# Kernel tuning notes

Hardware: AMD Instinct MI355X
Metric: run time of the kernel (lower is better)

The kernel has to match this reference:

```python
import jax, jax.numpy as jnp
import numpy as np
from jax import lax

GUARD_CELLS = 80
BG_CELLS = 80
ALPHA = 1.8
CFAR_UNITS = 1 + 2 * GUARD_CELLS + 2 * BG_CELLS          # 321
GUARD_UNITS = 2 * GUARD_CELLS + 1                         # 161
BG_AREA = CFAR_UNITS ** 2 - GUARD_UNITS ** 2              # background ring cell count
FRONT_DIV = (GUARD_UNITS ** 2) * ALPHA


def box_sum(x, k):
    """Same-padded KxK box sum over NCHW x (C=1), via separable 1D convs.

    Mathematically identical to a Conv2d with all-ones KxK kernel, zero bias,
    padding (k-1)//2 -- but O(N*K) instead of O(N*K^2).
    """
    p = (k - 1) // 2
    kh = jnp.ones((1, 1, k, 1), x.dtype)  # OIHW
    kw = jnp.ones((1, 1, 1, k), x.dtype)
    y = lax.conv_general_dilated(x, kh, window_strides=(1, 1), padding=[(p, p), (0, 0)])
    y = lax.conv_general_dilated(y, kw, window_strides=(1, 1), padding=[(0, 0), (p, p)])
    return y


def setup_inputs() -> dict:
    key = jax.random.key(0)
    x = jax.random.uniform(key, (4, 1, 1024, 1024), dtype=jnp.float32)
    return {"x": x}


def reference(x) -> jnp.ndarray:
    allsum = box_sum(x, CFAR_UNITS)            # conv1: 321x321 ones box
    front = box_sum(x, GUARD_UNITS)            # conv2: 161x161 ones box
    back = (allsum - front) / jnp.float32(BG_AREA)     # div1: 1x1 conv = scale
    front = front / jnp.float32(FRONT_DIV)             # div2: 1x1 conv = scale
    return front / back
```

## Files before the change

kernel.cpp:

```cpp
#include <hip/hip_runtime.h>
#include <hip/hip_bf16.h>


#define IMG 4
#define H 1024
#define W 1024
#define NSEG 32
#define SEGR 32
#define PADL 164
#define PADR 164
#define ROWLEN (PADL + W + PADR)

__global__ __launch_bounds__(256) void hbox_kernel(const float* __restrict__ x,
                                                   float* __restrict__ h161,
                                                   float* __restrict__ h321) {
    __shared__ float P[4][ROWLEN];
    const int wave = threadIdx.x >> 6;
    const int lane = threadIdx.x & 63;
    const int row  = (blockIdx.x << 2) + wave;

    const float4* xr = reinterpret_cast<const float4*>(x + (size_t)row * W);
    float v[16];
    {
        float4 a0 = xr[(lane << 2) + 0];
        float4 a1 = xr[(lane << 2) + 1];
        float4 a2 = xr[(lane << 2) + 2];
        float4 a3 = xr[(lane << 2) + 3];
        v[0]=a0.x; v[1]=a0.y; v[2]=a0.z; v[3]=a0.w;
        v[4]=a1.x; v[5]=a1.y; v[6]=a1.z; v[7]=a1.w;
        v[8]=a2.x; v[9]=a2.y; v[10]=a2.z; v[11]=a2.w;
        v[12]=a3.x; v[13]=a3.y; v[14]=a3.z; v[15]=a3.w;
    }
    float s = 0.f;
#pragma unroll
    for (int j = 0; j < 16; ++j) { s += v[j]; v[j] = s; }
    float t = s;
#pragma unroll
    for (int d = 1; d < 64; d <<= 1) {
        float u = __shfl_up(t, d, 64);
        if (lane >= d) t += u;
    }
    const float off = t - s;
#pragma unroll
    for (int j = 0; j < 16; ++j) v[j] += off;
    const float tot = __shfl(t, 63, 64);

    float* rowP = P[wave];
    float4* Pr = reinterpret_cast<float4*>(rowP + PADL);
    Pr[(lane << 2) + 0] = make_float4(v[0], v[1], v[2], v[3]);
    Pr[(lane << 2) + 1] = make_float4(v[4], v[5], v[6], v[7]);
    Pr[(lane << 2) + 2] = make_float4(v[8], v[9], v[10], v[11]);
    Pr[(lane << 2) + 3] = make_float4(v[12], v[13], v[14], v[15]);
    {
        float4* Pz = reinterpret_cast<float4*>(rowP);
        if (lane < 41) {
            Pz[lane]       = make_float4(0.f, 0.f, 0.f, 0.f);
            Pz[297 + lane] = make_float4(tot, tot, tot, tot);
        }
    }
    __syncthreads();

    const float* Pw = &P[wave][PADL];
    float* o161 = h161 + (size_t)row * W;
    float* o321 = h321 + (size_t)row * W;
#pragma unroll
    for (int k = 0; k < 16; ++k) {
        const int c = lane + (k << 6);
        const float s1 = Pw[c + 80]  - Pw[c - 81];
        const float s3 = Pw[c + 160] - Pw[c - 161];
        o161[c] = s1;
        o321[c] = s3;
    }
}

__global__ __launch_bounds__(256) void vscan_kernel(float* __restrict__ h161,
                                                    float* __restrict__ h321,
                                                    float* __restrict__ Btot) {
    const int bx  = blockIdx.x;
    const int img = bx >> 7;
    const int b7  = bx & 127;
    const int seg = b7 >> 2;
    const int cb  = b7 & 3;
    const int col = (cb << 8) + threadIdx.x;
    const int r0  = seg << 5;

    float* p = (blockIdx.y ? h321 : h161) + ((size_t)img << 20) + col;
    float sum = 0.f;
#pragma unroll
    for (int jj = 0; jj < SEGR; jj += 8) {
        float a[8];
#pragma unroll
        for (int j = 0; j < 8; ++j) a[j] = p[(size_t)(r0 + jj + j) << 10];
#pragma unroll
        for (int j = 0; j < 8; ++j) { sum += a[j]; a[j] = sum; }
#pragma unroll
        for (int j = 0; j < 8; ++j) p[(size_t)(r0 + jj + j) << 10] = a[j];
    }
    Btot[((((size_t)blockIdx.y << 2) + img) << 15) + ((size_t)seg << 10) + col] = sum;
}

__global__ __launch_bounds__(256) void segscan_kernel(const float* __restrict__ Btot,
                                                      float* __restrict__ SP) {
    const int t = blockIdx.x * 256 + threadIdx.x;
    const size_t base = ((size_t)(t >> 10) << 15) + (t & 1023);
    const float* b = Btot + base;
    float* sp = SP + base;
    float off = 0.f;
#pragma unroll
    for (int sg = 0; sg < NSEG; ++sg) {
        const float v = b[(size_t)sg << 10];
        sp[(size_t)sg << 10] = off;
        off += v;
    }
}

__global__ __launch_bounds__(512) void final_kernel(const float* __restrict__ g161,
                                                    const float* __restrict__ g321,
                                                    const float* __restrict__ SP,
                                                    float* __restrict__ out) {
    const int img = blockIdx.x >> 9;
    const int r   = ((blockIdx.x & 511) << 1) + (threadIdx.x >> 8);
    const int c4  = threadIdx.x & 255;

    const float4* P1 = reinterpret_cast<const float4*>(g161 + ((size_t)img << 20));
    const float4* P3 = reinterpret_cast<const float4*>(g321 + ((size_t)img << 20));
    const float4* SP1 = reinterpret_cast<const float4*>(SP) + ((size_t)img << 13);
    const float4* SP3 = reinterpret_cast<const float4*>(SP) + ((size_t)(IMG + img) << 13);

    const int hi1 = min(r + 80, H - 1),  lo1 = r - 81;
    const int hi3 = min(r + 160, H - 1), lo3 = r - 161;

    float4 f  = P1[((size_t)hi1 << 8) + c4];
    float4 fs = SP1[(((size_t)hi1 >> 5) << 8) + c4];
    float fx = f.x + fs.x, fy = f.y + fs.y, fz = f.z + fs.z, fw = f.w + fs.w;
    if (lo1 >= 0) {
        float4 g  = P1[((size_t)lo1 << 8) + c4];
        float4 gs = SP1[(((size_t)lo1 >> 5) << 8) + c4];
        fx -= g.x + gs.x; fy -= g.y + gs.y; fz -= g.z + gs.z; fw -= g.w + gs.w;
    }
    float4 a  = P3[((size_t)hi3 << 8) + c4];
    float4 as = SP3[(((size_t)hi3 >> 5) << 8) + c4];
    float ax = a.x + as.x, ay = a.y + as.y, az = a.z + as.z, aw = a.w + as.w;
    if (lo3 >= 0) {
        float4 g  = P3[((size_t)lo3 << 8) + c4];
        float4 gs = SP3[(((size_t)lo3 >> 5) << 8) + c4];
        ax -= g.x + gs.x; ay -= g.y + gs.y; az -= g.z + gs.z; aw -= g.w + gs.w;
    }

    const float SCALE = (float)(77120.0 / 46657.8);
    float4 o;
    o.x = SCALE * fx * __builtin_amdgcn_rcpf(ax - fx);
    o.y = SCALE * fy * __builtin_amdgcn_rcpf(ay - fy);
    o.z = SCALE * fz * __builtin_amdgcn_rcpf(az - fz);
    o.w = SCALE * fw * __builtin_amdgcn_rcpf(aw - fw);
    reinterpret_cast<float4*>(out + ((size_t)img << 20) + ((size_t)r << 10))[c4] = o;
}

extern "C" void kernel_launch(void* const* d_in, const int* in_sizes, int n_in,
                              void* d_out, int out_size, void* d_ws, size_t ws_size,
                              hipStream_t stream) {
    const float* x = (const float*)d_in[0];
    float* outp = (float*)d_out;
    float* h161 = (float*)d_ws;
    float* h321 = h161 + (size_t)IMG * H * W;
    float* Btot = h321 + (size_t)IMG * H * W;
    float* SPb  = Btot + (size_t)2 * IMG * NSEG * W;

    hbox_kernel<<<dim3((IMG * H) / 4), dim3(256), 0, stream>>>(x, h161, h321);
    vscan_kernel<<<dim3(512, 2), dim3(256), 0, stream>>>(h161, h321, Btot);
    segscan_kernel<<<dim3(32), dim3(256), 0, stream>>>(Btot, SPb);
    final_kernel<<<dim3(IMG * (H / 2)), dim3(512), 0, stream>>>(h161, h321, SPb, outp);
}
```

Baseline: 95.30 us.

## Store intermediate box sums as interleaved fp16 pairs to halve traffic

```diff
diff --git a/kernel.cpp b/kernel.cpp
--- a/kernel.cpp
+++ b/kernel.cpp
@@ -1,5 +1,6 @@
 #include <hip/hip_runtime.h>
 #include <hip/hip_bf16.h>
+#include <hip/hip_fp16.h>
 
 
 #define IMG 4
@@ -11,9 +12,11 @@
 #define PADR 164
 #define ROWLEN (PADL + W + PADR)
 
+struct h2x4 { __half2 v[4]; };
+struct f2x4 { float2  v[4]; };
+
 __global__ __launch_bounds__(256) void hbox_kernel(const float* __restrict__ x,
-                                                   float* __restrict__ h161,
-                                                   float* __restrict__ h321) {
+                                                   __half2* __restrict__ hs) {
     __shared__ float P[4][ROWLEN];
     const int wave = threadIdx.x >> 6;
     const int lane = threadIdx.x & 63;
@@ -61,21 +64,18 @@
     __syncthreads();
 
     const float* Pw = &P[wave][PADL];
-    float* o161 = h161 + (size_t)row * W;
-    float* o321 = h321 + (size_t)row * W;
+    __half2* oh = hs + (size_t)row * W;
 #pragma unroll
     for (int k = 0; k < 16; ++k) {
         const int c = lane + (k << 6);
         const float s1 = Pw[c + 80]  - Pw[c - 81];
         const float s3 = Pw[c + 160] - Pw[c - 161];
-        o161[c] = s1;
-        o321[c] = s3;
+        oh[c] = __floats2half2_rn(s1, s3);
     }
 }
 
-__global__ __launch_bounds__(256) void vscan_kernel(float* __restrict__ h161,
-                                                    float* __restrict__ h321,
-                                                    float* __restrict__ Btot) {
+__global__ __launch_bounds__(256) void vscan_kernel(__half2* __restrict__ hs,
+                                                    float2* __restrict__ Btot) {
     const int bx  = blockIdx.x;
     const int img = bx >> 7;
     const int b7  = bx & 127;
@@ -84,75 +84,85 @@
     const int col = (cb << 8) + threadIdx.x;
     const int r0  = seg << 5;
 
-    float* p = (blockIdx.y ? h321 : h161) + ((size_t)img << 20) + col;
-    float sum = 0.f;
+    __half2* p = hs + ((size_t)img << 20) + ((size_t)r0 << 10) + col;
+    float a1 = 0.f, a3 = 0.f;
 #pragma unroll
     for (int jj = 0; jj < SEGR; jj += 8) {
-        float a[8];
+        __half2 hv[8];
 #pragma unroll
-        for (int j = 0; j < 8; ++j) a[j] = p[(size_t)(r0 + jj + j) << 10];
+        for (int j = 0; j < 8; ++j) hv[j] = p[(size_t)(jj + j) << 10];
 #pragma unroll
-        for (int j = 0; j < 8; ++j) { sum += a[j]; a[j] = sum; }
-#pragma unroll
-        for (int j = 0; j < 8; ++j) p[(size_t)(r0 + jj + j) << 10] = a[j];
+        for (int j = 0; j < 8; ++j) {
+            const float2 f = __half22float2(hv[j]);
+            a1 += f.x; a3 += f.y;
+            p[(size_t)(jj + j) << 10] = __floats2half2_rn(a1, a3);
+        }
     }
-    Btot[((((size_t)blockIdx.y << 2) + img) << 15) + ((size_t)seg << 10) + col] = sum;
+    Btot[(((size_t)img * NSEG + seg) << 10) + col] = make_float2(a1, a3);
 }
 
-__global__ __launch_bounds__(256) void segscan_kernel(const float* __restrict__ Btot,
-                                                      float* __restrict__ SP) {
-    const int t = blockIdx.x * 256 + threadIdx.x;
-    const size_t base = ((size_t)(t >> 10) << 15) + (t & 1023);
-    const float* b = Btot + base;
-    float* sp = SP + base;
-    float off = 0.f;
+__global__ __launch_bounds__(256) void segscan_kernel(const float2* __restrict__ Btot,
+                                                      float2* __restrict__ SP) {
+    const int t   = blockIdx.x * 256 + threadIdx.x;
+    const int img = t >> 10;
+    const int col = t & 1023;
+    const float2* b  = Btot + ((size_t)img * NSEG << 10) + col;
+    float2*       sp = SP   + ((size_t)img * NSEG << 10) + col;
+    float o1 = 0.f, o3 = 0.f;
 #pragma unroll
     for (int sg = 0; sg < NSEG; ++sg) {
-        const float v = b[(size_t)sg << 10];
-        sp[(size_t)sg << 10] = off;
-        off += v;
+        const float2 v = b[(size_t)sg << 10];
+        sp[(size_t)sg << 10] = make_float2(o1, o3);
+        o1 += v.x; o3 += v.y;
     }
 }
 
-__global__ __launch_bounds__(512) void final_kernel(const float* __restrict__ g161,
-                                                    const float* __restrict__ g321,
-                                                    const float* __restrict__ SP,
+__global__ __launch_bounds__(512) void final_kernel(const __half2* __restrict__ hs,
+                                                    const float2* __restrict__ SP,
                                                     float* __restrict__ out) {
     const int img = blockIdx.x >> 9;
     const int r   = ((blockIdx.x & 511) << 1) + (threadIdx.x >> 8);
     const int c4  = threadIdx.x & 255;
+    const int cb  = c4 << 2;
 
-    const float4* P1 = reinterpret_cast<const float4*>(g161 + ((size_t)img << 20));
-    const float4* P3 = reinterpret_cast<const float4*>(g321 + ((size_t)img << 20));
-    const float4* SP1 = reinterpret_cast<const float4*>(SP) + ((size_t)img << 13);
-    const float4* SP3 = reinterpret_cast<const float4*>(SP) + ((size_t)(IMG + img) << 13);
+    const __half2* Hi = hs + ((size_t)img << 20);
+    const float2*  Si = SP + ((size_t)img * NSEG << 10);
 
     const int hi1 = min(r + 80, H - 1),  lo1 = r - 81;
     const int hi3 = min(r + 160, H - 1), lo3 = r - 161;
 
-    float4 f  = P1[((size_t)hi1 << 8) + c4];
-    float4 fs = SP1[(((size_t)hi1 >> 5) << 8) + c4];
-    float fx = f.x + fs.x, fy = f.y + fs.y, fz = f.z + fs.z, fw = f.w + fs.w;
+    float fx[4], ax[4];
+    {
+        const h2x4 Hh = *reinterpret_cast<const h2x4*>(Hi + ((size_t)hi1 << 10) + cb);
+        const f2x4 Sh = *reinterpret_cast<const f2x4*>(Si + (((size_t)hi1 >> 5) << 10) + cb);
+#pragma unroll
+        for (int i = 0; i < 4; ++i) fx[i] = __half22float2(Hh.v[i]).x + Sh.v[i].x;
+    }
     if (lo1 >= 0) {
-        float4 g  = P1[((size_t)lo1 << 8) + c4];
-        float4 gs = SP1[(((size_t)lo1 >> 5) << 8) + c4];
-        fx -= g.x + gs.x; fy -= g.y + gs.y; fz -= g.z + gs.z; fw -= g.w + gs.w;
+        const h2x4 Hl = *reinterpret_cast<const h2x4*>(Hi + ((size_t)lo1 << 10) + cb);
+        const f2x4 Sl = *reinterpret_cast<const f2x4*>(Si + (((size_t)lo1 >> 5) << 10) + cb);
+#pragma unroll
+        for (int i = 0; i < 4; ++i) fx[i] -= __half22float2(Hl.v[i]).x + Sl.v[i].x;
     }
-    float4 a  = P3[((size_t)hi3 << 8) + c4];
-    float4 as = SP3[(((size_t)hi3 >> 5) << 8) + c4];
-    float ax = a.x + as.x, ay = a.y + as.y, az = a.z + as.z, aw = a.w + as.w;
+    {
+        const h2x4 Hh = *reinterpret_cast<const h2x4*>(Hi + ((size_t)hi3 << 10) + cb);
+        const f2x4 Sh = *reinterpret_cast<const f2x4*>(Si + (((size_t)hi3 >> 5) << 10) + cb);
+#pragma unroll
+        for (int i = 0; i < 4; ++i) ax[i] = __half22float2(Hh.v[i]).y + Sh.v[i].y;
+    }
     if (lo3 >= 0) {
-        float4 g  = P3[((size_t)lo3 << 8) + c4];
-        float4 gs = SP3[(((size_t)lo3 >> 5) << 8) + c4];
-        ax -= g.x + gs.x; ay -= g.y + gs.y; az -= g.z + gs.z; aw -= g.w + gs.w;
+        const h2x4 Hl = *reinterpret_cast<const h2x4*>(Hi + ((size_t)lo3 << 10) + cb);
+        const f2x4 Sl = *reinterpret_cast<const f2x4*>(Si + (((size_t)lo3 >> 5) << 10) + cb);
+#pragma unroll
+        for (int i = 0; i < 4; ++i) ax[i] -= __half22float2(Hl.v[i]).y + Sl.v[i].y;
     }
 
     const float SCALE = (float)(77120.0 / 46657.8);
     float4 o;
-    o.x = SCALE * fx * __builtin_amdgcn_rcpf(ax - fx);
-    o.y = SCALE * fy * __builtin_amdgcn_rcpf(ay - fy);
-    o.z = SCALE * fz * __builtin_amdgcn_rcpf(az - fz);
-    o.w = SCALE * fw * __builtin_amdgcn_rcpf(aw - fw);
+    o.x = SCALE * fx[0] * __builtin_amdgcn_rcpf(ax[0] - fx[0]);
+    o.y = SCALE * fx[1] * __builtin_amdgcn_rcpf(ax[1] - fx[1]);
+    o.z = SCALE * fx[2] * __builtin_amdgcn_rcpf(ax[2] - fx[2]);
+    o.w = SCALE * fx[3] * __builtin_amdgcn_rcpf(ax[3] - fx[3]);
     reinterpret_cast<float4*>(out + ((size_t)img << 20) + ((size_t)r << 10))[c4] = o;
 }
 
@@ -161,13 +171,12 @@
                               hipStream_t stream) {
     const float* x = (const float*)d_in[0];
     float* outp = (float*)d_out;
-    float* h161 = (float*)d_ws;
-    float* h321 = h161 + (size_t)IMG * H * W;
-    float* Btot = h321 + (size_t)IMG * H * W;
-    float* SPb  = Btot + (size_t)2 * IMG * NSEG * W;
+    __half2* hs   = (__half2*)d_ws;
+    float2*  Btot = (float2*)((char*)d_ws + (size_t)IMG * H * W * 4);
+    float2*  SPb  = Btot + (size_t)IMG * NSEG * W;
 
-    hbox_kernel<<<dim3((IMG * H) / 4), dim3(256), 0, stream>>>(x, h161, h321);
-    vscan_kernel<<<dim3(512, 2), dim3(256), 0, stream>>>(h161, h321, Btot);
-    segscan_kernel<<<dim3(32), dim3(256), 0, stream>>>(Btot, SPb);
-    final_kernel<<<dim3(IMG * (H / 2)), dim3(512), 0, stream>>>(h161, h321, SPb, outp);
+    hbox_kernel<<<dim3((IMG * H) / 4), dim3(256), 0, stream>>>(x, hs);
+    vscan_kernel<<<dim3(512), dim3(256), 0, stream>>>(hs, Btot);
+    segscan_kernel<<<dim3(16), dim3(256), 0, stream>>>(Btot, SPb);
+    final_kernel<<<dim3(IMG * (H / 2)), dim3(512), 0, stream>>>(hs, SPb, outp);
 }
```

After: 111.7 us. +17.2%, slower.

## Fuse horizontal box sums with per-segment vertical scan in one kernel

Applied to the files above, without the earlier changes.

```diff
diff --git a/kernel.cpp b/kernel.cpp
--- a/kernel.cpp
+++ b/kernel.cpp
@@ -5,53 +5,57 @@
 #define IMG 4
 #define H 1024
 #define W 1024
-#define NSEG 32
-#define SEGR 32
+#define SEGR 8
+#define NSEG 128
 #define PADL 164
 #define PADR 164
 #define ROWLEN (PADL + W + PADR)
 
-__global__ __launch_bounds__(256) void hbox_kernel(const float* __restrict__ x,
-                                                   float* __restrict__ h161,
-                                                   float* __restrict__ h321) {
-    __shared__ float P[4][ROWLEN];
+__global__ __launch_bounds__(512) void hseg_kernel(const float* __restrict__ x,
+                                                   float* __restrict__ g161,
+                                                   float* __restrict__ g321,
+                                                   float* __restrict__ Btot) {
+    __shared__ float P[SEGR][ROWLEN];
     const int wave = threadIdx.x >> 6;
     const int lane = threadIdx.x & 63;
-    const int row  = (blockIdx.x << 2) + wave;
+    const int img  = blockIdx.x >> 7;
+    const int seg  = blockIdx.x & 127;
+    const int r0   = seg << 3;
 
-    const float4* xr = reinterpret_cast<const float4*>(x + (size_t)row * W);
-    float v[16];
     {
-        float4 a0 = xr[(lane << 2) + 0];
-        float4 a1 = xr[(lane << 2) + 1];
-        float4 a2 = xr[(lane << 2) + 2];
-        float4 a3 = xr[(lane << 2) + 3];
-        v[0]=a0.x; v[1]=a0.y; v[2]=a0.z; v[3]=a0.w;
-        v[4]=a1.x; v[5]=a1.y; v[6]=a1.z; v[7]=a1.w;
-        v[8]=a2.x; v[9]=a2.y; v[10]=a2.z; v[11]=a2.w;
-        v[12]=a3.x; v[13]=a3.y; v[14]=a3.z; v[15]=a3.w;
-    }
-    float s = 0.f;
+        const float4* xr = reinterpret_cast<const float4*>(
+            x + (((size_t)img << 10) + r0 + wave) * W);
+        float v[16];
+        {
+            float4 a0 = xr[(lane << 2) + 0];
+            float4 a1 = xr[(lane << 2) + 1];
+            float4 a2 = xr[(lane << 2) + 2];
+            float4 a3 = xr[(lane << 2) + 3];
+            v[0]=a0.x; v[1]=a0.y; v[2]=a0.z; v[3]=a0.w;
+            v[4]=a1.x; v[5]=a1.y; v[6]=a1.z; v[7]=a1.w;
+            v[8]=a2.x; v[9]=a2.y; v[10]=a2.z; v[11]=a2.w;
+            v[12]=a3.x; v[13]=a3.y; v[14]=a3.z; v[15]=a3.w;
+        }
+        float s = 0.f;
 #pragma unroll
-    for (int j = 0; j < 16; ++j) { s += v[j]; v[j] = s; }
-    float t = s;
+        for (int j = 0; j < 16; ++j) { s += v[j]; v[j] = s; }
+        float t = s;
 #pragma unroll
-    for (int d = 1; d < 64; d <<= 1) {
-        float u = __shfl_up(t, d, 64);
-        if (lane >= d) t += u;
-    }
-    const float off = t - s;
+        for (int d = 1; d < 64; d <<= 1) {
+            float u = __shfl_up(t, d, 64);
+            if (lane >= d) t += u;
+        }
+        const float off = t - s;
 #pragma unroll
-    for (int j = 0; j < 16; ++j) v[j] += off;
-    const float tot = __shfl(t, 63, 64);
+        for (int j = 0; j < 16; ++j) v[j] += off;
+        const float tot = __shfl(t, 63, 64);
 
-    float* rowP = P[wave];
-    float4* Pr = reinterpret_cast<float4*>(rowP + PADL);
-    Pr[(lane << 2) + 0] = make_float4(v[0], v[1], v[2], v[3]);
-    Pr[(lane << 2) + 1] = make_float4(v[4], v[5], v[6], v[7]);
-    Pr[(lane << 2) + 2] = make_float4(v[8], v[9], v[10], v[11]);
-    Pr[(lane << 2) + 3] = make_float4(v[12], v[13], v[14], v[15]);
-    {
+        float* rowP = P[wave];
+        float4* Pr = reinterpret_cast<float4*>(rowP + PADL);
+        Pr[(lane << 2) + 0] = make_float4(v[0], v[1], v[2], v[3]);
+        Pr[(lane << 2) + 1] = make_float4(v[4], v[5], v[6], v[7]);
+        Pr[(lane << 2) + 2] = make_float4(v[8], v[9], v[10], v[11]);
+        Pr[(lane << 2) + 3] = make_float4(v[12], v[13], v[14], v[15]);
         float4* Pz = reinterpret_cast<float4*>(rowP);
         if (lane < 41) {
             Pz[lane]       = make_float4(0.f, 0.f, 0.f, 0.f);
@@ -60,53 +64,38 @@
     }
     __syncthreads();
 
-    const float* Pw = &P[wave][PADL];
-    float* o161 = h161 + (size_t)row * W;
-    float* o321 = h321 + (size_t)row * W;
+    const int ca = threadIdx.x;
+    const int cc = threadIdx.x + 512;
+    float s1a = 0.f, s1b = 0.f, s3a = 0.f, s3b = 0.f;
+    float* o1 = g161 + ((size_t)img << 20) + ((size_t)r0 << 10);
+    float* o3 = g321 + ((size_t)img << 20) + ((size_t)r0 << 10);
+
 #pragma unroll
-    for (int k = 0; k < 16; ++k) {
-        const int c = lane + (k << 6);
-        const float s1 = Pw[c + 80]  - Pw[c - 81];
-        const float s3 = Pw[c + 160] - Pw[c - 161];
-        o161[c] = s1;
-        o321[c] = s3;
+    for (int j = 0; j < SEGR; ++j) {
+        const float* Pw = &P[j][PADL];
+        s1a += Pw[ca + 80]  - Pw[ca - 81];
+        s3a += Pw[ca + 160] - Pw[ca - 161];
+        s1b += Pw[cc + 80]  - Pw[cc - 81];
+        s3b += Pw[cc + 160] - Pw[cc - 161];
+        o1[(j << 10) + ca] = s1a;
+        o1[(j << 10) + cc] = s1b;
+        o3[(j << 10) + ca] = s3a;
+        o3[(j << 10) + cc] = s3b;
     }
-}
-
-__global__ __launch_bounds__(256) void vscan_kernel(float* __restrict__ h161,
-                                                    float* __restrict__ h321,
-                                                    float* __restrict__ Btot) {
-    const int bx  = blockIdx.x;
-    const int img = bx >> 7;
-    const int b7  = bx & 127;
-    const int seg = b7 >> 2;
-    const int cb  = b7 & 3;
-    const int col = (cb << 8) + threadIdx.x;
-    const int r0  = seg << 5;
-
-    float* p = (blockIdx.y ? h321 : h161) + ((size_t)img << 20) + col;
-    float sum = 0.f;
-#pragma unroll
-    for (int jj = 0; jj < SEGR; jj += 8) {
-        float a[8];
-#pragma unroll
-        for (int j = 0; j < 8; ++j) a[j] = p[(size_t)(r0 + jj + j) << 10];
-#pragma unroll
-        for (int j = 0; j < 8; ++j) { sum += a[j]; a[j] = sum; }
-#pragma unroll
-        for (int j = 0; j < 8; ++j) p[(size_t)(r0 + jj + j) << 10] = a[j];
-    }
-    Btot[((((size_t)blockIdx.y << 2) + img) << 15) + ((size_t)seg << 10) + col] = sum;
+    float* b1 = Btot + (((size_t)img * NSEG) + seg) * W;
+    float* b3 = Btot + (((size_t)(IMG + img) * NSEG) + seg) * W;
+    b1[ca] = s1a; b1[cc] = s1b;
+    b3[ca] = s3a; b3[cc] = s3b;
 }
 
 __global__ __launch_bounds__(256) void segscan_kernel(const float* __restrict__ Btot,
                                                       float* __restrict__ SP) {
     const int t = blockIdx.x * 256 + threadIdx.x;
-    const size_t base = ((size_t)(t >> 10) << 15) + (t & 1023);
+    const size_t base = (size_t)(t >> 10) * NSEG * W + (t & 1023);
     const float* b = Btot + base;
     float* sp = SP + base;
     float off = 0.f;
-#pragma unroll
+#pragma unroll 8
     for (int sg = 0; sg < NSEG; ++sg) {
         const float v = b[(size_t)sg << 10];
         sp[(size_t)sg << 10] = off;
@@ -124,26 +113,26 @@
 
     const float4* P1 = reinterpret_cast<const float4*>(g161 + ((size_t)img << 20));
     const float4* P3 = reinterpret_cast<const float4*>(g321 + ((size_t)img << 20));
-    const float4* SP1 = reinterpret_cast<const float4*>(SP) + ((size_t)img << 13);
-    const float4* SP3 = reinterpret_cast<const float4*>(SP) + ((size_t)(IMG + img) << 13);
+    const float4* SP1 = reinterpret_cast<const float4*>(SP) + ((size_t)img << 15);
+    const float4* SP3 = reinterpret_cast<const float4*>(SP) + ((size_t)(IMG + img) << 15);
 
     const int hi1 = min(r + 80, H - 1),  lo1 = r - 81;
     const int hi3 = min(r + 160, H - 1), lo3 = r - 161;
 
     float4 f  = P1[((size_t)hi1 << 8) + c4];
-    float4 fs = SP1[(((size_t)hi1 >> 5) << 8) + c4];
+    float4 fs = SP1[(((size_t)hi1 >> 3) << 8) + c4];
     float fx = f.x + fs.x, fy = f.y + fs.y, fz = f.z + fs.z, fw = f.w + fs.w;
     if (lo1 >= 0) {
         float4 g  = P1[((size_t)lo1 << 8) + c4];
-        float4 gs = SP1[(((size_t)lo1 >> 5) << 8) + c4];
+        float4 gs = SP1[(((size_t)lo1 >> 3) << 8) + c4];
         fx -= g.x + gs.x; fy -= g.y + gs.y; fz -= g.z + gs.z; fw -= g.w + gs.w;
     }
     float4 a  = P3[((size_t)hi3 << 8) + c4];
-    float4 as = SP3[(((size_t)hi3 >> 5) << 8) + c4];
+    float4 as = SP3[(((size_t)hi3 >> 3) << 8) + c4];
     float ax = a.x + as.x, ay = a.y + as.y, az = a.z + as.z, aw = a.w + as.w;
     if (lo3 >= 0) {
         float4 g  = P3[((size_t)lo3 << 8) + c4];
-        float4 gs = SP3[(((size_t)lo3 >> 5) << 8) + c4];
+        float4 gs = SP3[(((size_t)lo3 >> 3) << 8) + c4];
         ax -= g.x + gs.x; ay -= g.y + gs.y; az -= g.z + gs.z; aw -= g.w + gs.w;
     }
 
@@ -161,13 +150,12 @@
                               hipStream_t stream) {
     const float* x = (const float*)d_in[0];
     float* outp = (float*)d_out;
-    float* h161 = (float*)d_ws;
-    float* h321 = h161 + (size_t)IMG * H * W;
-    float* Btot = h321 + (size_t)IMG * H * W;
+    float* g161 = (float*)d_ws;
+    float* g321 = g161 + (size_t)IMG * H * W;
+    float* Btot = g321 + (size_t)IMG * H * W;
     float* SPb  = Btot + (size_t)2 * IMG * NSEG * W;
 
-    hbox_kernel<<<dim3((IMG * H) / 4), dim3(256), 0, stream>>>(x, h161, h321);
-    vscan_kernel<<<dim3(512, 2), dim3(256), 0, stream>>>(h161, h321, Btot);
+    hseg_kernel<<<dim3(IMG * NSEG), dim3(512), 0, stream>>>(x, g161, g321, Btot);
     segscan_kernel<<<dim3(32), dim3(256), 0, stream>>>(Btot, SPb);
-    final_kernel<<<dim3(IMG * (H / 2)), dim3(512), 0, stream>>>(h161, h321, SPb, outp);
+    final_kernel<<<dim3(IMG * (H / 2)), dim3(512), 0, stream>>>(g161, g321, SPb, outp);
 }
```

Result: no change. 96.96 us (+1.7%).
